# Kernel optimization log

Hardware: AMD Instinct MI355X
Metric: run time of the kernel (lower is better)

## Reference

```python
import jax, jax.numpy as jnp
import numpy as np

N_DIMS = 4
NEG_SLOPE = 0.01
ALPHA = 0.5

def leaky(v):
    return jnp.where(v > 0, v, NEG_SLOPE * v)

def gcn_conv(h, W, b, edge_index, n):
    """PyG GCNConv: add self-loops, symmetric normalization, then aggregate."""
    hw = h @ W  # [N, H]
    loops = jnp.arange(n, dtype=edge_index.dtype)
    src = jnp.concatenate([edge_index[0], loops])
    dst = jnp.concatenate([edge_index[1], loops])
    deg = jax.ops.segment_sum(jnp.ones_like(dst, dtype=hw.dtype), dst, num_segments=n)
    dinv = jnp.where(deg > 0, jax.lax.rsqrt(deg), 0.0)
    norm = dinv[src] * dinv[dst]  # [E+N]
    out = jax.ops.segment_sum(hw[src] * norm[:, None], dst, num_segments=n)
    return out + b

def setup_inputs() -> dict:
    key = jax.random.key(0)
    ks = jax.random.split(key, 8)
    N, IN, H, OUT, E = 50000, 512, 256, 512, 800000
    def kaiming(k, shape, fan_in):
        bound = np.sqrt(6.0 / fan_in)  # kaiming_uniform a=sqrt(5)-ish approx; gain sqrt(2)/sqrt(fan_in)*sqrt(3)
        bound = np.sqrt(2.0) * np.sqrt(3.0 / fan_in)
        return jax.random.uniform(k, shape, jnp.float32, -bound, bound)
    x = jax.random.normal(ks[0], (N, IN), jnp.float32)
    all_dim_edge_index = jax.random.randint(ks[1], (N_DIMS, 2, E), 0, N, jnp.int64)
    proj_mat = kaiming(ks[2], (N_DIMS, IN, H), IN)
    gcn_W = jax.random.uniform(ks[3], (N_DIMS, H, H), jnp.float32, -1, 1) * np.sqrt(1.0 / H)
    gcn_b = jnp.zeros((N_DIMS, H), jnp.float32)
    bilinear = kaiming(ks[4], (H, H), H)
    fan = H * N_DIMS
    inv_W = jax.random.uniform(ks[5], (fan, OUT), jnp.float32, -np.sqrt(1.0 / fan), np.sqrt(1.0 / fan))
    inv_b = jax.random.uniform(ks[6], (OUT,), jnp.float32, -np.sqrt(1.0 / fan), np.sqrt(1.0 / fan))
    return {"x": x, "all_dim_edge_index": all_dim_edge_index, "proj_mat": proj_mat,
            "gcn_W": gcn_W, "gcn_b": gcn_b, "bilinear": bilinear, "inv_W": inv_W, "inv_b": inv_b}

def reference(x, all_dim_edge_index, proj_mat, gcn_W, gcn_b, bilinear, inv_W, inv_b):
    n = x.shape[0]
    # per-dimension projection: [n_dims, N, H]
    dim_repr = leaky(jnp.einsum('ni,dih->dnh', x, proj_mat))
    # within-dimension GCN message passing (loop over small fixed n_dims)
    within_aggr = jnp.stack([
        gcn_conv(dim_repr[d], gcn_W[d], gcn_b[d], all_dim_edge_index[d], n)
        for d in range(N_DIMS)])
    # cross-dimension attention
    attention = jnp.einsum('aji,ik,bjk->ab', proj_mat, bilinear, proj_mat)
    attention = jax.nn.softmax(attention, axis=0)
    across_aggr = jnp.einsum('ab,anh->bnh', attention, dim_repr)
    new_dim_repr = ALPHA * within_aggr + (1.0 - ALPHA) * across_aggr  # [n_dims, N, H]
    concat = jnp.transpose(new_dim_repr, (1, 0, 2)).reshape(n, -1)  # [N, n_dims*H]
    return leaky(concat @ inv_W + inv_b)
```

## Files before the change

### kernel.cpp

```cpp
#include <hip/hip_runtime.h>
#include <math.h>

constexpr int N_NODES = 50000;
constexpr int IN_F    = 512;
constexpr int H_F     = 256;
constexpr int OUT_F   = 512;
constexpr int N_EDGE  = 800000;
constexpr int NDIM    = 4;
constexpr long NH     = (long)N_NODES * H_F;

#define LEAKY_SLOPE 0.01f

__device__ __forceinline__ float leaky_f(float v) { return v > 0.0f ? v : LEAKY_SLOPE * v; }

typedef __bf16 bf16x8 __attribute__((ext_vector_type(8)));
typedef float  f32x4  __attribute__((ext_vector_type(4)));

__device__ __forceinline__ void gload16(const void* g, void* s) {
  __builtin_amdgcn_global_load_lds(
      (const __attribute__((address_space(1))) void*)g,
      (__attribute__((address_space(3))) void*)s, 16, 0, 0);
}

template<bool AF32>
__global__ __launch_bounds__(256) void gemm_k(
    const float* __restrict__ Af, int ldaf,
    const __bf16* __restrict__ A1h, const __bf16* __restrict__ A1l, int lda1,
    const __bf16* __restrict__ A2h, const __bf16* __restrict__ A2l, int lda2, int kSplit,
    const __bf16* __restrict__ BhT, const __bf16* __restrict__ BlT,
    float* __restrict__ C, int ldc,
    const float* __restrict__ biasVec,
    __bf16* __restrict__ Oh, __bf16* __restrict__ Ol, int ldo,
    int M, int N, int K, int accumulate, int leaky)
{
  __shared__ __bf16 Ash[128][32];
  __shared__ __bf16 Asl[128][32];
  __shared__ __bf16 Bsh[128][32];
  __shared__ __bf16 Bsl[128][32];

  const int tid  = threadIdx.x;
  const int lane = tid & 63;
  const int wid  = tid >> 6;
  const int wm   = wid & 1;
  const int wn   = wid >> 1;
  const int l15  = lane & 15;
  const int quad = lane >> 4;
  const int col0 = blockIdx.x * 128;
  const int row0 = blockIdx.y * 128;

  f32x4 acc[4][4] = {};
  const int nkt = K >> 5;

  for (int kt = 0; kt < nkt; ++kt) {
    const int kk = kt << 5;
    __syncthreads();

    if constexpr (AF32) {
      #pragma unroll
      for (int p = 0; p < 4; ++p) {
        const int m = (tid >> 3) + p * 32;
        int row = row0 + m; row = row < M ? row : M - 1;
        const float4 v = *(const float4*)(Af + (size_t)row * ldaf + kk + (tid & 7) * 4);
        const float f[4] = {v.x, v.y, v.z, v.w};
        union { __bf16 b[4]; short4 s; } hh, ll;
        #pragma unroll
        for (int i = 0; i < 4; ++i) {
          const __bf16 hb = (__bf16)f[i];
          hh.b[i] = hb;
          ll.b[i] = (__bf16)(f[i] - (float)hb);
        }
        *(short4*)&Ash[m][(tid & 7) * 4] = hh.s;
        *(short4*)&Asl[m][(tid & 7) * 4] = ll.s;
      }
    } else {
      const __bf16* Ah; const __bf16* Al; int lda, k0;
      if (kk < kSplit) { Ah = A1h; Al = A1l; lda = lda1; k0 = kk; }
      else             { Ah = A2h; Al = A2l; lda = lda2; k0 = kk - kSplit; }
      #pragma unroll
      for (int p = 0; p < 2; ++p) {
        const int c = tid + p * 256;
        int row = row0 + (c >> 2); row = row < M ? row : M - 1;
        const size_t go = (size_t)row * lda + k0 + (c & 3) * 8;
        gload16(Ah + go, (__bf16*)Ash + (size_t)c * 8);
        gload16(Al + go, (__bf16*)Asl + (size_t)c * 8);
      }
    }
    #pragma unroll
    for (int p = 0; p < 2; ++p) {
      const int c = tid + p * 256;
      const int nn = col0 + (c >> 2);
      const size_t go = (size_t)nn * K + kk + (c & 3) * 8;
      gload16(BhT + go, (__bf16*)Bsh + (size_t)c * 8);
      gload16(BlT + go, (__bf16*)Bsl + (size_t)c * 8);
    }
    __syncthreads();

    bf16x8 ah[4], al[4], bh[4], bl[4];
    #pragma unroll
    for (int t = 0; t < 4; ++t) {
      ah[t] = *(const bf16x8*)&Ash[wm * 64 + t * 16 + l15][quad * 8];
      al[t] = *(const bf16x8*)&Asl[wm * 64 + t * 16 + l15][quad * 8];
      bh[t] = *(const bf16x8*)&Bsh[wn * 64 + t * 16 + l15][quad * 8];
      bl[t] = *(const bf16x8*)&Bsl[wn * 64 + t * 16 + l15][quad * 8];
    }
    #pragma unroll
    for (int mt = 0; mt < 4; ++mt)
      #pragma unroll
      for (int nt = 0; nt < 4; ++nt) {
        acc[mt][nt] = __builtin_amdgcn_mfma_f32_16x16x32_bf16(ah[mt], bh[nt], acc[mt][nt], 0, 0, 0);
        acc[mt][nt] = __builtin_amdgcn_mfma_f32_16x16x32_bf16(ah[mt], bl[nt], acc[mt][nt], 0, 0, 0);
        acc[mt][nt] = __builtin_amdgcn_mfma_f32_16x16x32_bf16(al[mt], bh[nt], acc[mt][nt], 0, 0, 0);
      }
  }

  #pragma unroll
  for (int mt = 0; mt < 4; ++mt)
    #pragma unroll
    for (int nt = 0; nt < 4; ++nt) {
      const int col = col0 + wn * 64 + nt * 16 + l15;
      const float bv = biasVec ? biasVec[col] : 0.0f;
      #pragma unroll
      for (int r = 0; r < 4; ++r) {
        const int row = row0 + wm * 64 + mt * 16 + quad * 4 + r;
        if (row < M) {
          float v = acc[mt][nt][r] + bv;
          if (accumulate) v += C[(size_t)row * ldc + col];
          if (leaky) v = leaky_f(v);
          if (Oh) {
            const __bf16 hv = (__bf16)v;
            Oh[(size_t)row * ldo + col] = hv;
            Ol[(size_t)row * ldo + col] = (__bf16)(v - (float)hv);
          } else {
            C[(size_t)row * ldc + col] = v;
          }
        }
      }
    }
}

__global__ void splitT_kernel(const float* __restrict__ B, __bf16* __restrict__ h,
                              __bf16* __restrict__ l, int Kd, int Nd, int total)
{
  int i = blockIdx.x * 256 + threadIdx.x;
  if (i >= total) return;
  int z   = i / (Kd * Nd);
  int rem = i - z * (Kd * Nd);
  int k = rem / Nd;
  int n = rem - k * Nd;
  float v = B[i];
  __bf16 hv = (__bf16)v;
  long o = (long)z * Kd * Nd + (long)n * Kd + k;
  h[o] = hv;
  l[o] = (__bf16)(v - (float)hv);
}

__global__ void splitA_kernel(const float* __restrict__ A, __bf16* __restrict__ h,
                              __bf16* __restrict__ l, long total)
{
  long i = (long)blockIdx.x * 256 + threadIdx.x;
  if (i >= total) return;
  float v = A[i];
  __bf16 hv = (__bf16)v;
  h[i] = hv;
  l[i] = (__bf16)(v - (float)hv);
}

__global__ void bcat_kernel(const float* __restrict__ invW, const float* __restrict__ att,
                            __bf16* __restrict__ h, __bf16* __restrict__ l)
{
  int i = blockIdx.x * 256 + threadIdx.x;
  if (i >= NDIM * OUT_F * 512) return;
  int d   = i >> 18;
  int rem = i & 262143;
  int n = rem >> 9;
  int k = rem & 511;
  float v;
  if (k < H_F) {
    v = invW[(long)(d * H_F + k) * OUT_F + n];
  } else {
    float s = 0.f;
    #pragma unroll
    for (int b = 0; b < 4; ++b)
      s += att[d * 4 + b] * invW[(long)(b * H_F + (k - H_F)) * OUT_F + n];
    v = 0.5f * s;
  }
  __bf16 hv = (__bf16)v;
  h[i] = hv;
  l[i] = (__bf16)(v - (float)hv);
}

__global__ void deg_count_kernel(const int* __restrict__ edges, int* __restrict__ cnt, int E)
{
  int i = blockIdx.x * 256 + threadIdx.x;
  if (i >= NDIM * E) return;
  int d = i / E;
  int e = i - d * E;
  int t = edges[(long)d * 2 * E + E + e];
  atomicAdd(&cnt[d * N_NODES + t], 1);
}

__global__ __launch_bounds__(1024) void scan_kernel(const int* __restrict__ cnt,
                                                    int* __restrict__ row_start,
                                                    float* __restrict__ dinv)
{
  const int d    = blockIdx.x;
  const int tid  = threadIdx.x;
  const int lane = tid & 63;
  const int wid  = tid >> 6;
  __shared__ int wsum[16];
  __shared__ int carry_s;
  if (tid == 0) carry_s = 0;
  __syncthreads();
  for (int base = 0; base < N_NODES; base += 1024) {
    int i = base + tid;
    int v = (i < N_NODES) ? cnt[d * N_NODES + i] : 0;
    if (i < N_NODES) dinv[d * N_NODES + i] = sqrtf(0.5f / (float)(v + 1));
    int incl = v;
    #pragma unroll
    for (int off = 1; off < 64; off <<= 1) {
      int nb = __shfl_up(incl, off, 64);
      if (lane >= off) incl += nb;
    }
    if (lane == 63) wsum[wid] = incl;
    __syncthreads();
    if (wid == 0 && lane < 16) {
      int s = wsum[lane];
      #pragma unroll
      for (int off = 1; off < 16; off <<= 1) {
        int nb = __shfl_up(s, off, 16);
        if (lane >= off) s += nb;
      }
      wsum[lane] = s;
    }
    __syncthreads();
    int waveoff = (wid == 0) ? 0 : wsum[wid - 1];
    if (i < N_NODES) row_start[d * (N_NODES + 1) + i] = carry_s + waveoff + incl - v;
    __syncthreads();
    if (tid == 1023) carry_s += wsum[15];
    __syncthreads();
  }
  if (tid == 0) row_start[d * (N_NODES + 1) + N_NODES] = carry_s;
}

__global__ void fill_kernel(const int* __restrict__ edges, const int* __restrict__ row_start,
                            int* __restrict__ fill_cnt, int* __restrict__ csr_src, int E)
{
  int i = blockIdx.x * 256 + threadIdx.x;
  if (i >= NDIM * E) return;
  int d = i / E;
  int e = i - d * E;
  int s = edges[(long)d * 2 * E + e];
  int t = edges[(long)d * 2 * E + E + e];
  int pos = row_start[d * (N_NODES + 1) + t] + atomicAdd(&fill_cnt[d * N_NODES + t], 1);
  csr_src[(long)d * E + pos] = s;
}

__global__ __launch_bounds__(256) void gather_aggr_kernel(
    const float* __restrict__ hw, const int* __restrict__ csr_src,
    const int* __restrict__ row_start, const float* __restrict__ dinv,
    const float* __restrict__ bias, __bf16* __restrict__ Wh, __bf16* __restrict__ Wl)
{
  const int n = blockIdx.x * 4 + (threadIdx.x >> 6);
  const int lane = threadIdx.x & 63;
  const float dt = dinv[n];
  const float sl = dt * dt;
  const float4 b = *(const float4*)(bias + lane * 4);
  const float4 h = *(const float4*)(hw + (size_t)n * H_F + lane * 4);
  float4 a0 = make_float4(0.5f * b.x + sl * h.x, 0.5f * b.y + sl * h.y,
                          0.5f * b.z + sl * h.z, 0.5f * b.w + sl * h.w);
  float4 a1 = make_float4(0.f, 0.f, 0.f, 0.f);
  const int beg = row_start[n];
  const int end = row_start[n + 1];
  int j = beg;
  for (; j + 2 <= end; j += 2) {
    const int s0 = csr_src[j];
    const int s1 = csr_src[j + 1];
    const float nm0 = dt * dinv[s0];
    const float nm1 = dt * dinv[s1];
    const float4 v0 = *(const float4*)(hw + (size_t)s0 * H_F + lane * 4);
    const float4 v1 = *(const float4*)(hw + (size_t)s1 * H_F + lane * 4);
    a0.x = fmaf(nm0, v0.x, a0.x); a0.y = fmaf(nm0, v0.y, a0.y);
    a0.z = fmaf(nm0, v0.z, a0.z); a0.w = fmaf(nm0, v0.w, a0.w);
    a1.x = fmaf(nm1, v1.x, a1.x); a1.y = fmaf(nm1, v1.y, a1.y);
    a1.z = fmaf(nm1, v1.z, a1.z); a1.w = fmaf(nm1, v1.w, a1.w);
  }
  if (j < end) {
    const int s0 = csr_src[j];
    const float nm0 = dt * dinv[s0];
    const float4 v0 = *(const float4*)(hw + (size_t)s0 * H_F + lane * 4);
    a0.x = fmaf(nm0, v0.x, a0.x); a0.y = fmaf(nm0, v0.y, a0.y);
    a0.z = fmaf(nm0, v0.z, a0.z); a0.w = fmaf(nm0, v0.w, a0.w);
  }
  const float av[4] = {a0.x + a1.x, a0.y + a1.y, a0.z + a1.z, a0.w + a1.w};
  union { __bf16 b[4]; short4 s; } H, L;
  #pragma unroll
  for (int i = 0; i < 4; ++i) {
    const __bf16 hv = (__bf16)av[i];
    H.b[i] = hv;
    L.b[i] = (__bf16)(av[i] - (float)hv);
  }
  *(short4*)(Wh + (size_t)n * H_F + lane * 4) = H.s;
  *(short4*)(Wl + (size_t)n * H_F + lane * 4) = L.s;
}

__global__ void att_dot_kernel(const float* __restrict__ T, const float* __restrict__ P,
                               float* __restrict__ out16)
{
  const int a = blockIdx.x >> 2;
  const int b = blockIdx.x & 3;
  const float* ta = T + (long)a * (IN_F * H_F);
  const float* pb = P + (long)b * (IN_F * H_F);
  float s = 0.f;
  for (int i = threadIdx.x; i < IN_F * H_F; i += 256) s += ta[i] * pb[i];
  #pragma unroll
  for (int off = 32; off > 0; off >>= 1) s += __shfl_down(s, off, 64);
  __shared__ float red[4];
  if ((threadIdx.x & 63) == 0) red[threadIdx.x >> 6] = s;
  __syncthreads();
  if (threadIdx.x == 0) out16[blockIdx.x] = red[0] + red[1] + red[2] + red[3];
}

__global__ void att_softmax_kernel(const float* __restrict__ raw, float* __restrict__ att)
{
  int b = threadIdx.x;
  if (b < 4) {
    float r0 = raw[b], r1 = raw[4 + b], r2 = raw[8 + b], r3 = raw[12 + b];
    float m = fmaxf(fmaxf(r0, r1), fmaxf(r2, r3));
    float e0 = expf(r0 - m), e1 = expf(r1 - m), e2 = expf(r2 - m), e3 = expf(r3 - m);
    float inv = 1.0f / (e0 + e1 + e2 + e3);
    att[b] = e0 * inv; att[4 + b] = e1 * inv; att[8 + b] = e2 * inv; att[12 + b] = e3 * inv;
  }
}

extern "C" void kernel_launch(void* const* d_in, const int* in_sizes, int n_in,
                              void* d_out, int out_size, void* d_ws, size_t ws_size,
                              hipStream_t stream)
{
  const float* x     = (const float*)d_in[0];
  const int*   edges = (const int*)d_in[1];
  const float* proj  = (const float*)d_in[2];
  const float* gcnW  = (const float*)d_in[3];
  const float* gcnB  = (const float*)d_in[4];
  const float* bil   = (const float*)d_in[5];
  const float* invW  = (const float*)d_in[6];
  const float* invB  = (const float*)d_in[7];
  float* out = (float*)d_out;

  float* HWB       = (float*)d_ws;
  float* dinv      = HWB + NH;
  float* Tbuf      = dinv + NDIM * N_NODES;
  float* att_raw   = Tbuf + (long)NDIM * IN_F * H_F;
  float* att       = att_raw + 16;
  int*   cnt       = (int*)(att + 16);
  int*   fill_cnt  = cnt + NDIM * N_NODES;
  int*   row_start = fill_cnt + NDIM * N_NODES;
  int*   csr_src   = row_start + NDIM * (N_NODES + 1);
  __bf16* projTh   = (__bf16*)(csr_src + (long)NDIM * N_EDGE);
  __bf16* projTl   = projTh + (long)NDIM * IN_F * H_F;
  __bf16* gcnWTh   = projTl + (long)NDIM * IN_F * H_F;
  __bf16* gcnWTl   = gcnWTh + (long)NDIM * H_F * H_F;
  __bf16* bcatTh   = gcnWTl + (long)NDIM * H_F * H_F;
  __bf16* bcatTl   = bcatTh + (long)NDIM * OUT_F * 512;
  __bf16* bilTh    = bcatTl + (long)NDIM * OUT_F * 512;
  __bf16* bilTl    = bilTh + (long)H_F * H_F;
  __bf16* Rh       = bilTl + (long)H_F * H_F;
  __bf16* Rl       = Rh + NH;
  __bf16* WBh      = Rl + NH;
  __bf16* WBl      = WBh + NH;
  __bf16* xh       = WBl + NH;
  __bf16* xl       = xh + (long)N_NODES * IN_F;
  const size_t need_x = (size_t)((char*)(xl + (long)N_NODES * IN_F) - (char*)d_ws);
  const bool XS = ws_size >= need_x;

  const int MBL = (N_NODES + 127) / 128;

  hipMemsetAsync(cnt, 0, (size_t)2 * NDIM * N_NODES * sizeof(int), stream);
  deg_count_kernel<<<(NDIM * N_EDGE + 255) / 256, 256, 0, stream>>>(edges, cnt, N_EDGE);
  scan_kernel<<<NDIM, 1024, 0, stream>>>(cnt, row_start, dinv);
  fill_kernel<<<(NDIM * N_EDGE + 255) / 256, 256, 0, stream>>>(edges, row_start, fill_cnt,
                                                               csr_src, N_EDGE);

  splitT_kernel<<<(NDIM * IN_F * H_F + 255) / 256, 256, 0, stream>>>(
      proj, projTh, projTl, IN_F, H_F, NDIM * IN_F * H_F);
  splitT_kernel<<<(NDIM * H_F * H_F + 255) / 256, 256, 0, stream>>>(
      gcnW, gcnWTh, gcnWTl, H_F, H_F, NDIM * H_F * H_F);
  splitT_kernel<<<(H_F * H_F + 255) / 256, 256, 0, stream>>>(
      bil, bilTh, bilTl, H_F, H_F, H_F * H_F);

  for (int a = 0; a < NDIM; ++a)
    gemm_k<true><<<dim3(H_F / 128, IN_F / 128), 256, 0, stream>>>(
        proj + (long)a * IN_F * H_F, H_F,
        nullptr, nullptr, 0, nullptr, nullptr, 0, 0,
        bilTh, bilTl,
        Tbuf + (long)a * IN_F * H_F, H_F,
        nullptr, nullptr, nullptr, 0,
        IN_F, H_F, H_F, 0, 0);
  att_dot_kernel<<<16, 256, 0, stream>>>(Tbuf, proj, att_raw);
  att_softmax_kernel<<<1, 64, 0, stream>>>(att_raw, att);
  bcat_kernel<<<(NDIM * OUT_F * 512 + 255) / 256, 256, 0, stream>>>(invW, att, bcatTh, bcatTl);

  if (XS)
    splitA_kernel<<<(int)(((long)N_NODES * IN_F + 255) / 256), 256, 0, stream>>>(
        x, xh, xl, (long)N_NODES * IN_F);

  for (int d = 0; d < NDIM; ++d) {
    if (XS)
      gemm_k<false><<<dim3(H_F / 128, MBL), 256, 0, stream>>>(
          nullptr, 0,
          xh, xl, IN_F, xh, xl, IN_F, IN_F,
          projTh + (long)d * IN_F * H_F, projTl + (long)d * IN_F * H_F,
          nullptr, 0, nullptr,
          Rh, Rl, H_F,
          N_NODES, H_F, IN_F, 0, 1);
    else
      gemm_k<true><<<dim3(H_F / 128, MBL), 256, 0, stream>>>(
          x, IN_F,
          nullptr, nullptr, 0, nullptr, nullptr, 0, 0,
          projTh + (long)d * IN_F * H_F, projTl + (long)d * IN_F * H_F,
          nullptr, 0, nullptr,
          Rh, Rl, H_F,
          N_NODES, H_F, IN_F, 0, 1);

    gemm_k<false><<<dim3(H_F / 128, MBL), 256, 0, stream>>>(
        nullptr, 0,
        Rh, Rl, H_F, Rh, Rl, H_F, H_F,
        gcnWTh + (long)d * H_F * H_F, gcnWTl + (long)d * H_F * H_F,
        HWB, H_F, nullptr,
        nullptr, nullptr, 0,
        N_NODES, H_F, H_F, 0, 0);

    gather_aggr_kernel<<<N_NODES / 4, 256, 0, stream>>>(
        HWB, csr_src + (long)d * N_EDGE, row_start + d * (N_NODES + 1),
        dinv + d * N_NODES, gcnB + d * H_F, WBh, WBl);

    gemm_k<false><<<dim3(OUT_F / 128, MBL), 256, 0, stream>>>(
        nullptr, 0,
        WBh, WBl, H_F, Rh, Rl, H_F, H_F,
        bcatTh + (long)d * OUT_F * 512, bcatTl + (long)d * OUT_F * 512,
        out, OUT_F, (d == 0) ? invB : nullptr,
        nullptr, nullptr, 0,
        N_NODES, OUT_F, 512, (d == 0) ? 0 : 1, (d == NDIM - 1) ? 1 : 0);
  }

  (void)in_sizes; (void)n_in; (void)out_size; (void)ws_size;
}
```

Measured before the change: 2.927 ms.

## Double-buffer GEMM LDS tiles, swizzle, XCD remap, merge final projection GEMMs

The GEMM kernel now double-buffers its LDS tiles so global loads for the next K-slice overlap the MFMA work on the current one. It also applies an XOR swizzle to the LDS layout to cut bank conflicts and remaps workgroups across XCDs for better L2 locality. When the workspace allows, per-dimension R and WB buffers are kept for all four dimensions, and the four accumulate-into-output GEMMs are merged into one K=2048 GEMM through a pointer table. The merge removes three read-modify-write passes over the output, at the cost of extra workspace and a more complex A-tile addressing scheme.

```diff
diff --git a/kernel.cpp b/kernel.cpp
--- a/kernel.cpp
+++ b/kernel.cpp
@@ -16,6 +16,8 @@
 typedef __bf16 bf16x8 __attribute__((ext_vector_type(8)));
 typedef float  f32x4  __attribute__((ext_vector_type(4)));
 
+struct PtrTab { const __bf16* h[8]; const __bf16* l[8]; };
+
 __device__ __forceinline__ void gload16(const void* g, void* s) {
   __builtin_amdgcn_global_load_lds(
       (const __attribute__((address_space(1))) void*)g,
@@ -25,18 +27,17 @@
 template<bool AF32>
 __global__ __launch_bounds__(256) void gemm_k(
     const float* __restrict__ Af, int ldaf,
-    const __bf16* __restrict__ A1h, const __bf16* __restrict__ A1l, int lda1,
-    const __bf16* __restrict__ A2h, const __bf16* __restrict__ A2l, int lda2, int kSplit,
-    const __bf16* __restrict__ BhT, const __bf16* __restrict__ BlT,
+    PtrTab at, int lda,
+    const __bf16* __restrict__ BhT, const __bf16* __restrict__ BlT, int ldb,
     float* __restrict__ C, int ldc,
     const float* __restrict__ biasVec,
     __bf16* __restrict__ Oh, __bf16* __restrict__ Ol, int ldo,
     int M, int N, int K, int accumulate, int leaky)
 {
-  __shared__ __bf16 Ash[128][32];
-  __shared__ __bf16 Asl[128][32];
-  __shared__ __bf16 Bsh[128][32];
-  __shared__ __bf16 Bsl[128][32];
+  __shared__ __bf16 AshF[2][4096];
+  __shared__ __bf16 AslF[2][4096];
+  __shared__ __bf16 BshF[2][4096];
+  __shared__ __bf16 BslF[2][4096];
 
   const int tid  = threadIdx.x;
   const int lane = tid & 63;
@@ -45,63 +46,106 @@
   const int wn   = wid >> 1;
   const int l15  = lane & 15;
   const int quad = lane >> 4;
-  const int col0 = blockIdx.x * 128;
-  const int row0 = blockIdx.y * 128;
+
+  const int nwg = (int)(gridDim.x * gridDim.y);
+  const int hw  = (int)(blockIdx.y * gridDim.x + blockIdx.x);
+  const int xcd = hw & 7, idx = hw >> 3;
+  const int q8 = nwg >> 3, r8 = nwg & 7;
+  const int wk = (xcd < r8 ? xcd * (q8 + 1) : r8 * (q8 + 1) + (xcd - r8) * q8) + idx;
+  const int col0 = (wk % (int)gridDim.x) * 128;
+  const int row0 = (wk / (int)gridDim.x) * 128;
 
   f32x4 acc[4][4] = {};
   const int nkt = K >> 5;
 
+  float4 areg[4];
+
+  auto stageB = [&](int buf, int kt) {
+    const int kb = kt << 5;
+    #pragma unroll
+    for (int p = 0; p < 2; ++p) {
+      const int c  = tid + p * 256;
+      const int rr = c >> 2;
+      const int sw = ((c & 3) ^ ((rr >> 1) & 3)) * 8;
+      const size_t go = (size_t)(col0 + rr) * ldb + kb + sw;
+      gload16(BhT + go, &BshF[buf][c * 8]);
+      gload16(BlT + go, &BslF[buf][c * 8]);
+    }
+  };
+  auto stageA = [&](int buf, int kt) {
+    const int ch = kt >> 3;
+    const __bf16* __restrict__ Ah = at.h[ch];
+    const __bf16* __restrict__ Al = at.l[ch];
+    const int ka = (kt & 7) << 5;
+    #pragma unroll
+    for (int p = 0; p < 2; ++p) {
+      const int c  = tid + p * 256;
+      const int rr = c >> 2;
+      const int sw = ((c & 3) ^ ((rr >> 1) & 3)) * 8;
+      int row = row0 + rr; row = row < M ? row : M - 1;
+      const size_t go = (size_t)row * lda + ka + sw;
+      gload16(Ah + go, &AshF[buf][c * 8]);
+      gload16(Al + go, &AslF[buf][c * 8]);
+    }
+  };
+  auto loadA32 = [&](int kt) {
+    #pragma unroll
+    for (int p = 0; p < 4; ++p) {
+      const int m = (tid >> 3) + p * 32;
+      int row = row0 + m; row = row < M ? row : M - 1;
+      areg[p] = *(const float4*)(Af + (size_t)row * ldaf + (kt << 5) + (tid & 7) * 4);
+    }
+  };
+  auto writeA32 = [&](int buf) {
+    const int q16 = (tid & 7) >> 1;
+    const int sub = (tid & 1) * 4;
+    #pragma unroll
+    for (int p = 0; p < 4; ++p) {
+      const int m = (tid >> 3) + p * 32;
+      const float f[4] = {areg[p].x, areg[p].y, areg[p].z, areg[p].w};
+      union { __bf16 b[4]; short4 s; } hh, ll;
+      #pragma unroll
+      for (int i = 0; i < 4; ++i) {
+        const __bf16 hb = (__bf16)f[i];
+        hh.b[i] = hb;
+        ll.b[i] = (__bf16)(f[i] - (float)hb);
+      }
+      const int off = m * 32 + ((q16 ^ ((m >> 1) & 3)) * 8) + sub;
+      *(short4*)&AshF[buf][off] = hh.s;
+      *(short4*)&AslF[buf][off] = ll.s;
+    }
+  };
+
+  if constexpr (AF32) {
+    loadA32(0);
+    stageB(0, 0);
+    writeA32(0);
+  } else {
+    stageA(0, 0);
+    stageB(0, 0);
+  }
+  __syncthreads();
+
+  int cur = 0;
   for (int kt = 0; kt < nkt; ++kt) {
-    const int kk = kt << 5;
-    __syncthreads();
-
+    const bool more = (kt + 1 < nkt);
     if constexpr (AF32) {
-      #pragma unroll
-      for (int p = 0; p < 4; ++p) {
-        const int m = (tid >> 3) + p * 32;
-        int row = row0 + m; row = row < M ? row : M - 1;
-        const float4 v = *(const float4*)(Af + (size_t)row * ldaf + kk + (tid & 7) * 4);
-        const float f[4] = {v.x, v.y, v.z, v.w};
-        union { __bf16 b[4]; short4 s; } hh, ll;
-        #pragma unroll
-        for (int i = 0; i < 4; ++i) {
-          const __bf16 hb = (__bf16)f[i];
-          hh.b[i] = hb;
-          ll.b[i] = (__bf16)(f[i] - (float)hb);
-        }
-        *(short4*)&Ash[m][(tid & 7) * 4] = hh.s;
-        *(short4*)&Asl[m][(tid & 7) * 4] = ll.s;
-      }
+      if (more) { loadA32(kt + 1); stageB(cur ^ 1, kt + 1); }
     } else {
-      const __bf16* Ah; const __bf16* Al; int lda, k0;
-      if (kk < kSplit) { Ah = A1h; Al = A1l; lda = lda1; k0 = kk; }
-      else             { Ah = A2h; Al = A2l; lda = lda2; k0 = kk - kSplit; }
-      #pragma unroll
-      for (int p = 0; p < 2; ++p) {
-        const int c = tid + p * 256;
-        int row = row0 + (c >> 2); row = row < M ? row : M - 1;
-        const size_t go = (size_t)row * lda + k0 + (c & 3) * 8;
-        gload16(Ah + go, (__bf16*)Ash + (size_t)c * 8);
-        gload16(Al + go, (__bf16*)Asl + (size_t)c * 8);
-      }
-    }
-    #pragma unroll
-    for (int p = 0; p < 2; ++p) {
-      const int c = tid + p * 256;
-      const int nn = col0 + (c >> 2);
-      const size_t go = (size_t)nn * K + kk + (c & 3) * 8;
-      gload16(BhT + go, (__bf16*)Bsh + (size_t)c * 8);
-      gload16(BlT + go, (__bf16*)Bsl + (size_t)c * 8);
-    }
-    __syncthreads();
+      if (more) { stageA(cur ^ 1, kt + 1); stageB(cur ^ 1, kt + 1); }
+    }
 
     bf16x8 ah[4], al[4], bh[4], bl[4];
     #pragma unroll
     for (int t = 0; t < 4; ++t) {
-      ah[t] = *(const bf16x8*)&Ash[wm * 64 + t * 16 + l15][quad * 8];
-      al[t] = *(const bf16x8*)&Asl[wm * 64 + t * 16 + l15][quad * 8];
-      bh[t] = *(const bf16x8*)&Bsh[wn * 64 + t * 16 + l15][quad * 8];
-      bl[t] = *(const bf16x8*)&Bsl[wn * 64 + t * 16 + l15][quad * 8];
+      const int ar = wm * 64 + t * 16 + l15;
+      const int br = wn * 64 + t * 16 + l15;
+      const int as = ar * 32 + ((quad ^ ((ar >> 1) & 3)) * 8);
+      const int bs = br * 32 + ((quad ^ ((br >> 1) & 3)) * 8);
+      ah[t] = *(const bf16x8*)&AshF[cur][as];
+      al[t] = *(const bf16x8*)&AslF[cur][as];
+      bh[t] = *(const bf16x8*)&BshF[cur][bs];
+      bl[t] = *(const bf16x8*)&BslF[cur][bs];
     }
     #pragma unroll
     for (int mt = 0; mt < 4; ++mt)
@@ -111,6 +155,12 @@
         acc[mt][nt] = __builtin_amdgcn_mfma_f32_16x16x32_bf16(ah[mt], bl[nt], acc[mt][nt], 0, 0, 0);
         acc[mt][nt] = __builtin_amdgcn_mfma_f32_16x16x32_bf16(al[mt], bh[nt], acc[mt][nt], 0, 0, 0);
       }
+
+    if constexpr (AF32) {
+      if (more) writeA32(cur ^ 1);
+    }
+    __syncthreads();
+    cur ^= 1;
   }
 
   #pragma unroll
@@ -185,8 +235,9 @@
     v = 0.5f * s;
   }
   __bf16 hv = (__bf16)v;
-  h[i] = hv;
-  l[i] = (__bf16)(v - (float)hv);
+  long o = (long)n * (NDIM * 512) + d * 512 + k;
+  h[o] = hv;
+  l[o] = (__bf16)(v - (float)hv);
 }
 
 __global__ void deg_count_kernel(const int* __restrict__ edges, int* __restrict__ cnt, int E)
@@ -363,16 +414,24 @@
   __bf16* bcatTl   = bcatTh + (long)NDIM * OUT_F * 512;
   __bf16* bilTh    = bcatTl + (long)NDIM * OUT_F * 512;
   __bf16* bilTl    = bilTh + (long)H_F * H_F;
-  __bf16* Rh       = bilTl + (long)H_F * H_F;
-  __bf16* Rl       = Rh + NH;
-  __bf16* WBh      = Rl + NH;
-  __bf16* WBl      = WBh + NH;
-  __bf16* xh       = WBl + NH;
-  __bf16* xl       = xh + (long)N_NODES * IN_F;
-  const size_t need_x = (size_t)((char*)(xl + (long)N_NODES * IN_F) - (char*)d_ws);
-  const bool XS = ws_size >= need_x;
+  __bf16* dynBase  = bilTl + (long)H_F * H_F;
+
+  const size_t base_bytes  = (size_t)((char*)dynBase - (char*)d_ws);
+  const size_t need_merged = base_bytes + (size_t)16 * NH * sizeof(__bf16);
+  const size_t need_xs     = need_merged + (size_t)2 * N_NODES * IN_F * sizeof(__bf16);
+  const bool MERGED = ws_size >= need_merged;
+  const bool XS     = ws_size >= need_xs;
+  const int  RD     = MERGED ? NDIM : 1;
+
+  __bf16* Rh  = dynBase;
+  __bf16* Rl  = Rh + (long)RD * NH;
+  __bf16* WBh = Rl + (long)RD * NH;
+  __bf16* WBl = WBh + (long)RD * NH;
+  __bf16* xh  = WBl + (long)RD * NH;
+  __bf16* xl  = xh + (long)N_NODES * IN_F;
 
   const int MBL = (N_NODES + 127) / 128;
+  PtrTab empty{};
 
   hipMemsetAsync(cnt, 0, (size_t)2 * NDIM * N_NODES * sizeof(int), stream);
   deg_count_kernel<<<(NDIM * N_EDGE + 255) / 256, 256, 0, stream>>>(edges, cnt, N_EDGE);
@@ -390,8 +449,8 @@
   for (int a = 0; a < NDIM; ++a)
     gemm_k<true><<<dim3(H_F / 128, IN_F / 128), 256, 0, stream>>>(
         proj + (long)a * IN_F * H_F, H_F,
-        nullptr, nullptr, 0, nullptr, nullptr, 0, 0,
-        bilTh, bilTl,
+        empty, 0,
+        bilTh, bilTl, H_F,
         Tbuf + (long)a * IN_F * H_F, H_F,
         nullptr, nullptr, nullptr, 0,
         IN_F, H_F, H_F, 0, 0);
@@ -403,44 +462,82 @@
     splitA_kernel<<<(int)(((long)N_NODES * IN_F + 255) / 256), 256, 0, stream>>>(
         x, xh, xl, (long)N_NODES * IN_F);
 
+  if (MERGED) {
+    for (int d = 0; d < NDIM; ++d) {
+      if (XS) {
+        PtrTab t{};
+        for (int c = 0; c < 8; ++c) { t.h[c] = xh + (c & 1) * 256; t.l[c] = xl + (c & 1) * 256; }
+        gemm_k<false><<<dim3(H_F / 128, MBL), 256, 0, stream>>>(
+            nullptr, 0, t, IN_F,
+            projTh + (long)d * IN_F * H_F, projTl + (long)d * IN_F * H_F, IN_F,
+            nullptr, 0, nullptr,
+            Rh + (long)d * NH, Rl + (long)d * NH, H_F,
+            N_NODES, H_F, IN_F, 0, 1);
+      } else {
+        gemm_k<true><<<dim3(H_F / 128, MBL), 256, 0, stream>>>(
+            x, IN_F, empty, 0,
+            projTh + (long)d * IN_F * H_F, projTl + (long)d * IN_F * H_F, IN_F,
+            nullptr, 0, nullptr,
+            Rh + (long)d * NH, Rl + (long)d * NH, H_F,
+            N_NODES, H_F, IN_F, 0, 1);
+      }
+    }
+  }
+
   for (int d = 0; d < NDIM; ++d) {
-    if (XS)
-      gemm_k<false><<<dim3(H_F / 128, MBL), 256, 0, stream>>>(
-          nullptr, 0,
-          xh, xl, IN_F, xh, xl, IN_F, IN_F,
-          projTh + (long)d * IN_F * H_F, projTl + (long)d * IN_F * H_F,
+    const long rslot = MERGED ? d : 0;
+    if (!MERGED) {
+      gemm_k<true><<<dim3(H_F / 128, MBL), 256, 0, stream>>>(
+          x, IN_F, empty, 0,
+          projTh + (long)d * IN_F * H_F, projTl + (long)d * IN_F * H_F, IN_F,
           nullptr, 0, nullptr,
           Rh, Rl, H_F,
           N_NODES, H_F, IN_F, 0, 1);
-    else
-      gemm_k<true><<<dim3(H_F / 128, MBL), 256, 0, stream>>>(
-          x, IN_F,
-          nullptr, nullptr, 0, nullptr, nullptr, 0, 0,
-          projTh + (long)d * IN_F * H_F, projTl + (long)d * IN_F * H_F,
-          nullptr, 0, nullptr,
-          Rh, Rl, H_F,
-          N_NODES, H_F, IN_F, 0, 1);
-
-    gemm_k<false><<<dim3(H_F / 128, MBL), 256, 0, stream>>>(
-        nullptr, 0,
-        Rh, Rl, H_F, Rh, Rl, H_F, H_F,
-        gcnWTh + (long)d * H_F * H_F, gcnWTl + (long)d * H_F * H_F,
-        HWB, H_F, nullptr,
-        nullptr, nullptr, 0,
-        N_NODES, H_F, H_F, 0, 0);
-
+    }
+    {
+      PtrTab t{};
+      for (int c = 0; c < 8; ++c) { t.h[c] = Rh + rslot * NH; t.l[c] = Rl + rslot * NH; }
+      gemm_k<false><<<dim3(H_F / 128, MBL), 256, 0, stream>>>(
+          nullptr, 0, t, H_F,
+          gcnWTh + (long)d * H_F * H_F, gcnWTl + (long)d * H_F * H_F, H_F,
+          HWB, H_F, nullptr,
+          nullptr, nullptr, 0,
+          N_NODES, H_F, H_F, 0, 0);
+    }
     gather_aggr_kernel<<<N_NODES / 4, 256, 0, stream>>>(
         HWB, csr_src + (long)d * N_EDGE, row_start + d * (N_NODES + 1),
-        dinv + d * N_NODES, gcnB + d * H_F, WBh, WBl);
-
+        dinv + d * N_NODES, gcnB + d * H_F,
+        WBh + rslot * NH, WBl + rslot * NH);
+
+    if (!MERGED) {
+      PtrTab t{};
+      for (int c = 0; c < 8; ++c) {
+        t.h[c] = (c & 1) ? Rh : WBh;
+        t.l[c] = (c & 1) ? Rl : WBl;
+      }
+      gemm_k<false><<<dim3(OUT_F / 128, MBL), 256, 0, stream>>>(
+          nullptr, 0, t, H_F,
+          bcatTh + (long)d * 512, bcatTl + (long)d * 512, NDIM * 512,
+          out, OUT_F, (d == 0) ? invB : nullptr,
+          nullptr, nullptr, 0,
+          N_NODES, OUT_F, 512, (d == 0) ? 0 : 1, (d == NDIM - 1) ? 1 : 0);
+    }
+  }
+
+  if (MERGED) {
+    PtrTab t{};
+    for (int c = 0; c < 8; ++c) {
+      const long dd = c >> 1;
+      t.h[c] = (c & 1) ? Rh + dd * NH : WBh + dd * NH;
+      t.l[c] = (c & 1) ? Rl + dd * NH : WBl + dd * NH;
+    }
     gemm_k<false><<<dim3(OUT_F / 128, MBL), 256, 0, stream>>>(
-        nullptr, 0,
-        WBh, WBl, H_F, Rh, Rl, H_F, H_F,
-        bcatTh + (long)d * OUT_F * 512, bcatTl + (long)d * OUT_F * 512,
-        out, OUT_F, (d == 0) ? invB : nullptr,
+        nullptr, 0, t, H_F,
+        bcatTh, bcatTl, NDIM * 512,
+        out, OUT_F, invB,
         nullptr, nullptr, 0,
-        N_NODES, OUT_F, 512, (d == 0) ? 0 : 1, (d == NDIM - 1) ? 1 : 0);
-  }
-
-  (void)in_sizes; (void)n_in; (void)out_size; (void)ws_size;
-}
+        N_NODES, OUT_F, NDIM * 512, 0, 1);
+  }
+
+  (void)in_sizes; (void)n_in; (void)out_size;
+}
```

Measured after the change: 2.739 ms. 6.4% less time.
